# Optimization experiments

Measured on AMD Instinct MI355X. Metric: run time of the kernel, lower is better.

Reference implementation:

```python
import jax, jax.numpy as jnp
import numpy as np

N = 100000   # nodes
E = 1600000  # edges
B = 4096     # graphs
F_IN = 92
H = 51       # hidden_channels
ED = 10      # edge_dim
T = 7        # num_timesteps

def _p(key, shape, scale=0.1):
    return scale * jax.random.normal(key, shape, dtype=jnp.float32)

def setup_inputs():
    key = jax.random.key(0)
    ks = jax.random.split(key, 20)
    return {
        "x": jax.random.normal(ks[0], (N, F_IN), dtype=jnp.float32),
        "edge_index": jax.random.randint(ks[1], (2, E), 0, N),
        "edge_attr": jax.random.normal(ks[2], (E, ED), dtype=jnp.float32),
        "batch": jnp.sort(jax.random.randint(ks[3], (N,), 0, B)),
        "W1": _p(ks[4], (F_IN, H)), "b1": jnp.zeros((H,), jnp.float32),
        "We1": _p(ks[5], (H + ED, H)),
        "att_l": _p(ks[6], (H,)), "att_r": _p(ks[7], (H,)),
        "We2": _p(ks[8], (H, H)), "gate_bias": jnp.zeros((H,), jnp.float32),
        "Wih1": _p(ks[9], (H, 3 * H)), "bih1": jnp.zeros((3 * H,), jnp.float32),
        "Whh1": _p(ks[10], (H, 3 * H)), "bhh1": jnp.zeros((3 * H,), jnp.float32),
        "Wm": _p(ks[11], (H, H)),
        "att_src": _p(ks[12], (H,)), "att_dst": _p(ks[13], (H,)),
        "mol_bias": jnp.zeros((H,), jnp.float32),
        "Wih2": _p(ks[14], (H, 3 * H)), "bih2": jnp.zeros((3 * H,), jnp.float32),
        "Whh2": _p(ks[15], (H, 3 * H)), "bhh2": jnp.zeros((3 * H,), jnp.float32),
        "W2": _p(ks[16], (H, 1)), "b2": jnp.zeros((1,), jnp.float32),
    }

def _lrelu(v):
    return jax.nn.leaky_relu(v, 0.01)

def _seg_softmax(a, idx, num):
    # scatter-softmax over segments (PyG softmax with 1e-16 denom eps)
    m = jax.ops.segment_max(a, idx, num_segments=num)
    e = jnp.exp(a - m[idx])
    s = jax.ops.segment_sum(e, idx, num_segments=num)
    return e / (s[idx] + 1e-16)

def _gru(xin, h, Wih, bih, Whh, bhh):
    # torch.nn.GRUCell, gate order r, z, n
    gi = xin @ Wih + bih
    gh = h @ Whh + bhh
    ir, iz, inn = jnp.split(gi, 3, axis=-1)
    hr, hz, hn = jnp.split(gh, 3, axis=-1)
    r = jax.nn.sigmoid(ir + hr)
    z = jax.nn.sigmoid(iz + hz)
    n = jnp.tanh(inn + r * hn)
    return (1.0 - z) * n + z * h

def reference(x, edge_index, edge_attr, batch, W1, b1, We1, att_l, att_r, We2,
              gate_bias, Wih1, bih1, Whh1, bhh1, Wm, att_src, att_dst, mol_bias,
              Wih2, bih2, Whh2, bhh2, W2, b2):
    src, dst = edge_index[0], edge_index[1]
    # AttentiveFP.lin1 + leaky_relu
    x = _lrelu(x @ W1 + b1)                                        # (N, H)
    # GATEConv: edge-conditioned attention, aggregate to dst
    xe = _lrelu(jnp.concatenate([x[src], edge_attr], axis=-1) @ We1)  # (E, H)
    a = _lrelu(xe @ att_l + x[dst] @ att_r)                        # (E,)
    alpha = _seg_softmax(a, dst, N)
    h = jax.ops.segment_sum((xe @ We2) * alpha[:, None], dst, num_segments=N) + gate_bias
    h = jax.nn.elu(h)                                              # dropout off (eval)
    x = jax.nn.relu(_gru(h, x, Wih1, bih1, Whh1, bhh1))            # (N, H)
    # molecule readout: GATConv over bipartite (nodes -> graphs) edges (arange(N), batch)
    out = jax.nn.relu(jax.ops.segment_sum(x, batch, num_segments=B))  # (B, H)
    xl = x @ Wm                                                    # (N, H), constant over t
    al = xl @ att_src                                              # (N,)
    for _ in range(T):
        ar = (out @ Wm) @ att_dst                                  # (B,)
        a = _lrelu(al + ar[batch])
        alpha = _seg_softmax(a, batch, B)
        hm = jax.ops.segment_sum(xl * alpha[:, None], batch, num_segments=B) + mol_bias
        hm = jax.nn.elu(hm)
        out = jax.nn.relu(_gru(hm, out, Wih2, bih2, Whh2, bhh2))
    return out @ W2 + b2                                           # (B, 1)
```

## Files before the change

kernel.cpp:

```cpp
#include <hip/hip_runtime.h>
#include <stdint.h>

#define NN 100000
#define NE 1600000
#define NB 4096
#define FIN 92
#define H 51
#define H3 153
#define TSTEPS 7
#define SCAN_B 391

__device__ __align__(16) float g_x1[(size_t)NN * 52 + 64];
__device__ __align__(16) float g_p[(size_t)NN * 52 + 64];
__device__ float g_xr[NN];
__device__ float g_agg[(size_t)NN * H + 64];
__device__ float g_x2[(size_t)NN * H + 64];
__device__ float g_xl[(size_t)NN * H + 64];
__device__ float g_al[NN];
__device__ int   g_gs[NB + 2];
__device__ float g_wg1[H * H * 8];
__device__ float g_bg1[64 * 8];
__device__ float g_wg2[H * H * 8];
__device__ float g_bg2[64 * 8];
__device__ float g_wv[64];
__device__ int   g_cnt[NN];
__device__ int   g_rp[NN + 1];
__device__ int   g_cur[NN];
__device__ int   g_src[NE + 4];
__device__ __align__(16) float g_eac[(size_t)NE * 12 + 16];
__device__ int   g_bsum[512];
__device__ int   g_boff[512];

__device__ __forceinline__ float lrelu(float v) { return v > 0.f ? v : 0.01f * v; }
__device__ __forceinline__ float elu1(float v) { return v > 0.f ? v : expm1f(v); }
__device__ __forceinline__ float sigm(float v) { return 1.f / (1.f + __expf(-v)); }

__device__ __forceinline__ float bflo(uint32_t w) { union { uint32_t u; float f; } c; c.u = w << 16; return c.f; }
__device__ __forceinline__ float bfhi(uint32_t w) { union { uint32_t u; float f; } c; c.u = w & 0xffff0000u; return c.f; }
__device__ __forceinline__ uint32_t f2bf(float f) {
    uint32_t u = __float_as_uint(f);
    return (u + 0x7FFFu + ((u >> 16) & 1u)) >> 16;
}

__device__ __forceinline__ float wave_sum(float v) {
    v += __shfl_xor(v, 32, 64);
    v += __shfl_xor(v, 16, 64);
    v += __shfl_xor(v, 8, 64);
    v += __shfl_xor(v, 4, 64);
    v += __shfl_xor(v, 2, 64);
    v += __shfl_xor(v, 1, 64);
    return v;
}
__device__ __forceinline__ void wave_sum4(float& a, float& b, float& c, float& d) {
    a += __shfl_xor(a, 32, 64); b += __shfl_xor(b, 32, 64); c += __shfl_xor(c, 32, 64); d += __shfl_xor(d, 32, 64);
    a += __shfl_xor(a, 16, 64); b += __shfl_xor(b, 16, 64); c += __shfl_xor(c, 16, 64); d += __shfl_xor(d, 16, 64);
    a += __shfl_xor(a, 8, 64);  b += __shfl_xor(b, 8, 64);  c += __shfl_xor(c, 8, 64);  d += __shfl_xor(d, 8, 64);
    a += __shfl_xor(a, 4, 64);  b += __shfl_xor(b, 4, 64);  c += __shfl_xor(c, 4, 64);  d += __shfl_xor(d, 4, 64);
    a += __shfl_xor(a, 2, 64);  b += __shfl_xor(b, 2, 64);  c += __shfl_xor(c, 2, 64);  d += __shfl_xor(d, 2, 64);
    a += __shfl_xor(a, 1, 64);  b += __shfl_xor(b, 1, 64);  c += __shfl_xor(c, 1, 64);  d += __shfl_xor(d, 1, 64);
}

__device__ __forceinline__ float d4(float acc, float4 t, float4 wv) {
    return fmaf(t.x, wv.x, fmaf(t.y, wv.y, fmaf(t.z, wv.z, fmaf(t.w, wv.w, acc))));
}

__global__ __launch_bounds__(256) void k_init(const int* __restrict__ batch) {
    int n = blockIdx.x * 256 + threadIdx.x;
    if (n >= NN) return;
    g_cnt[n] = 0;
    int bn = batch[n];
    int bp = (n == 0) ? -1 : batch[n - 1];
    for (int b = bp + 1; b <= bn; ++b) g_gs[b] = n;
    if (n == NN - 1) for (int b = bn + 1; b <= NB; ++b) g_gs[b] = NN;
}

__global__ void k_prep(const float* __restrict__ Wih1, const float* __restrict__ bih1,
                       const float* __restrict__ Whh1, const float* __restrict__ bhh1,
                       const float* __restrict__ Wih2, const float* __restrict__ bih2,
                       const float* __restrict__ Whh2, const float* __restrict__ bhh2,
                       const float* __restrict__ Wm, const float* __restrict__ ad) {
    int id = blockIdx.x * 256 + threadIdx.x;
    int which = 0;
    const float *Wih, *bih, *Whh, *bhh;
    if (id < H * H) {
        which = 0; Wih = Wih1; bih = bih1; Whh = Whh1; bhh = bhh1;
    } else if (id < 2 * H * H) {
        which = 1; id -= H * H; Wih = Wih2; bih = bih2; Whh = Whh2; bhh = bhh2;
    } else {
        int k = id - 2 * H * H;
        if (k < 64) {
            float a = 0.f;
            if (k < H) for (int j = 0; j < H; ++j) a = fmaf(Wm[k * H + j], ad[j], a);
            g_wv[k] = a;
        }
        return;
    }
    float* Wg = which ? g_wg2 : g_wg1;
    float* bg = which ? g_bg2 : g_bg1;
    int k = id / H, j = id - k * H;
    float* o = Wg + (size_t)id * 8;
    o[0] = Wih[k * H3 + j];
    o[1] = Wih[k * H3 + H + j];
    o[2] = Wih[k * H3 + 2 * H + j];
    o[3] = Whh[k * H3 + j];
    o[4] = Whh[k * H3 + H + j];
    o[5] = Whh[k * H3 + 2 * H + j];
    o[6] = 0.f; o[7] = 0.f;
    if (id < H) {
        float* ob = bg + (size_t)id * 8;
        ob[0] = bih[id]; ob[1] = bih[H + id]; ob[2] = bih[2 * H + id];
        ob[3] = bhh[id]; ob[4] = bhh[H + id]; ob[5] = bhh[2 * H + id];
        ob[6] = 0.f; ob[7] = 0.f;
    }
}

__global__ __launch_bounds__(256) void k_count(const int* __restrict__ ei) {
    int e = blockIdx.x * 256 + threadIdx.x;
    if (e >= NE) return;
    atomicAdd(&g_cnt[ei[NE + e]], 1);
}

__global__ __launch_bounds__(256) void k_scan1() {
    __shared__ int sm[256];
    int tid = threadIdx.x;
    int i = blockIdx.x * 256 + tid;
    sm[tid] = (i < NN) ? g_cnt[i] : 0;
    __syncthreads();
#pragma unroll
    for (int off = 1; off < 256; off <<= 1) {
        int t = (tid >= off) ? sm[tid - off] : 0;
        __syncthreads();
        sm[tid] += t;
        __syncthreads();
    }
    if (i < NN) g_rp[i + 1] = sm[tid];
    if (tid == 255) g_bsum[blockIdx.x] = sm[255];
}

__global__ void k_scan2() {
    __shared__ int sm[512];
    int tid = threadIdx.x;
    sm[tid] = (tid < SCAN_B) ? g_bsum[tid] : 0;
    __syncthreads();
#pragma unroll
    for (int off = 1; off < 512; off <<= 1) {
        int t = (tid >= off) ? sm[tid - off] : 0;
        __syncthreads();
        sm[tid] += t;
        __syncthreads();
    }
    if (tid < SCAN_B) g_boff[tid] = (tid == 0) ? 0 : sm[tid - 1];
}

__global__ __launch_bounds__(256) void k_scan3() {
    int i = blockIdx.x * 256 + threadIdx.x;
    if (i >= NN) return;
    int v = g_rp[i + 1] + g_boff[blockIdx.x];
    g_rp[i + 1] = v;
    if (i == 0) { g_rp[0] = 0; g_cur[0] = 0; }
    if (i + 1 < NN) g_cur[i + 1] = v;
}

__global__ __launch_bounds__(256) void k_fill(const int* __restrict__ ei, const float* __restrict__ ea) {
    int e = blockIdx.x * 256 + threadIdx.x;
    if (e >= NE) return;
    int d = ei[NE + e];
    int pos = atomicAdd(&g_cur[d], 1);
    g_src[pos] = ei[e];
    const float2* s2 = (const float2*)(ea + (size_t)e * 10);
    float2 v0 = s2[0], v1 = s2[1], v2 = s2[2], v3 = s2[3], v4 = s2[4];
    float2* d2 = (float2*)(g_eac + (size_t)pos * 12);
    d2[0] = v0; d2[1] = v1; d2[2] = v2; d2[3] = v3; d2[4] = v4;
    d2[5] = make_float2(0.f, 0.f);
}

__global__ __launch_bounds__(256, 3) void k_lin1(const float* __restrict__ x, const float* __restrict__ W1,
                                                 const float* __restrict__ b1, const float* __restrict__ attr_,
                                                 const float* __restrict__ We1) {
    int n = blockIdx.x * 256 + threadIdx.x;
    if (n >= NN) return;
    const float4* xq4 = (const float4*)(x + (size_t)n * FIN);
    float acc[H];
#pragma unroll
    for (int h = 0; h < H; ++h) acc[h] = 0.f;
#pragma unroll 1
    for (int q = 0; q < FIN / 4; ++q) {
        float4 v = xq4[q];
        const float* wr = W1 + (4 * q) * H;
#pragma unroll
        for (int h = 0; h < H; ++h)
            acc[h] = fmaf(v.x, wr[h], fmaf(v.y, wr[H + h], fmaf(v.z, wr[2 * H + h], fmaf(v.w, wr[3 * H + h], acc[h]))));
    }
    float xrv = 0.f;
    float* xo = g_x1 + (size_t)n * 52;
#pragma unroll
    for (int h = 0; h < H; ++h) {
        float v = lrelu(acc[h] + b1[h]);
        acc[h] = v;
        xo[h] = v;
        xrv = fmaf(v, attr_[h], xrv);
    }
    xo[H] = 0.f;
    g_xr[n] = xrv;
    float* po = g_p + (size_t)n * 52;
#pragma unroll 1
    for (int h = 0; h < H; ++h) {
        float ph = 0.f;
#pragma unroll
        for (int k = 0; k < H; ++k) ph = fmaf(acc[k], We1[k * H + h], ph);
        po[h] = ph;
    }
    po[H] = 0.f;
}

#define MKE(q) make_float4( \
    (4*(q)+0) < 10 ? We1[(51 + 4*(q)+0) * H + lj] : 0.f, \
    (4*(q)+1) < 10 ? We1[(51 + 4*(q)+1) * H + lj] : 0.f, \
    (4*(q)+2) < 10 ? We1[(51 + 4*(q)+2) * H + lj] : 0.f, \
    (4*(q)+3) < 10 ? We1[(51 + 4*(q)+3) * H + lj] : 0.f)

__global__ __launch_bounds__(256, 4) void k_gate(const float* __restrict__ We1, const float* __restrict__ attl) {
    int lane = threadIdx.x & 63;
    int lj = lane < H ? lane : H - 1;
    int n = __builtin_amdgcn_readfirstlane(blockIdx.x * 4 + (threadIdx.x >> 6));
    float4 eq0 = MKE(0), eq1 = MKE(1), eq2 = MKE(2);
    float attlv = attl[lj];
    float xrd = g_xr[n];
    int rs = g_rp[n], re = g_rp[n + 1];
    float accH = 0.f, den = 0.f;
    int nb = (re - rs) >> 2;
    int idx = rs;
    float pv0 = 0.f, pv1 = 0.f, pv2 = 0.f, pv3 = 0.f;
    if (nb > 0) {
        int s0 = __builtin_amdgcn_readfirstlane(g_src[idx]);
        int s1 = __builtin_amdgcn_readfirstlane(g_src[idx + 1]);
        int s2 = __builtin_amdgcn_readfirstlane(g_src[idx + 2]);
        int s3 = __builtin_amdgcn_readfirstlane(g_src[idx + 3]);
        pv0 = g_p[(size_t)s0 * 52 + lane];
        pv1 = g_p[(size_t)s1 * 52 + lane];
        pv2 = g_p[(size_t)s2 * 52 + lane];
        pv3 = g_p[(size_t)s3 * 52 + lane];
    }
#pragma unroll 1
    for (int blk = 0; blk < nb; ++blk) {
        int ci = idx;
        float cp0 = pv0, cp1 = pv1, cp2 = pv2, cp3 = pv3;
        idx += 4;
        if (blk + 1 < nb) {
            int s0 = __builtin_amdgcn_readfirstlane(g_src[idx]);
            int s1 = __builtin_amdgcn_readfirstlane(g_src[idx + 1]);
            int s2 = __builtin_amdgcn_readfirstlane(g_src[idx + 2]);
            int s3 = __builtin_amdgcn_readfirstlane(g_src[idx + 3]);
            pv0 = g_p[(size_t)s0 * 52 + lane];
            pv1 = g_p[(size_t)s1 * 52 + lane];
            pv2 = g_p[(size_t)s2 * 52 + lane];
            pv3 = g_p[(size_t)s3 * 52 + lane];
        }
        const float4* ep0 = (const float4*)(g_eac + (size_t)ci * 12);
        const float4* ep1 = (const float4*)(g_eac + (size_t)(ci + 1) * 12);
        const float4* ep2 = (const float4*)(g_eac + (size_t)(ci + 2) * 12);
        const float4* ep3 = (const float4*)(g_eac + (size_t)(ci + 3) * 12);
        float xe0 = cp0, xe1 = cp1, xe2 = cp2, xe3 = cp3;
        xe0 = d4(xe0, ep0[0], eq0); xe0 = d4(xe0, ep0[1], eq1); xe0 = d4(xe0, ep0[2], eq2);
        xe1 = d4(xe1, ep1[0], eq0); xe1 = d4(xe1, ep1[1], eq1); xe1 = d4(xe1, ep1[2], eq2);
        xe2 = d4(xe2, ep2[0], eq0); xe2 = d4(xe2, ep2[1], eq1); xe2 = d4(xe2, ep2[2], eq2);
        xe3 = d4(xe3, ep3[0], eq0); xe3 = d4(xe3, ep3[1], eq1); xe3 = d4(xe3, ep3[2], eq2);
        float l0 = lrelu(xe0), l1 = lrelu(xe1), l2 = lrelu(xe2), l3 = lrelu(xe3);
        float p0 = (lane < H) ? l0 * attlv : 0.f;
        float p1 = (lane < H) ? l1 * attlv : 0.f;
        float p2 = (lane < H) ? l2 * attlv : 0.f;
        float p3 = (lane < H) ? l3 * attlv : 0.f;
        wave_sum4(p0, p1, p2, p3);
        float e0 = __expf(lrelu(p0 + xrd));
        float e1 = __expf(lrelu(p1 + xrd));
        float e2 = __expf(lrelu(p2 + xrd));
        float e3 = __expf(lrelu(p3 + xrd));
        accH = fmaf(e0, l0, accH); den += e0;
        accH = fmaf(e1, l1, accH); den += e1;
        accH = fmaf(e2, l2, accH); den += e2;
        accH = fmaf(e3, l3, accH); den += e3;
    }
    for (; idx < re; ++idx) {
        int s0 = __builtin_amdgcn_readfirstlane(g_src[idx]);
        float pvs = g_p[(size_t)s0 * 52 + lane];
        const float4* ep0 = (const float4*)(g_eac + (size_t)idx * 12);
        float xe0 = pvs;
        xe0 = d4(xe0, ep0[0], eq0); xe0 = d4(xe0, ep0[1], eq1); xe0 = d4(xe0, ep0[2], eq2);
        float l0 = lrelu(xe0);
        float a0 = wave_sum((lane < H) ? l0 * attlv : 0.f);
        float e0 = __expf(lrelu(a0 + xrd));
        accH = fmaf(e0, l0, accH); den += e0;
    }
    if (lane < H) g_agg[(size_t)n * H + lane] = accH / (den + 1e-16f);
}

__global__ __launch_bounds__(256) void k_gategru(const float* __restrict__ We2, const float* __restrict__ gb,
                                                 const float* __restrict__ Wm, const float* __restrict__ asrc) {
    __shared__ float lbc[4][52][8];
    int w = threadIdx.x >> 6;
    int lane = threadIdx.x & 63;
    int lj = lane < H ? lane : H - 1;
    int base = __builtin_amdgcn_readfirstlane(blockIdx.x * 32 + w * 8);
    float xj[8];
#pragma unroll
    for (int m = 0; m < 8; ++m) xj[m] = g_x1[(size_t)(base + m) * 52 + lane];
    float ac[8];
#pragma unroll
    for (int m = 0; m < 8; ++m) ac[m] = 0.f;
#pragma unroll 2
    for (int k = 0; k < H; ++k) {
        float wv = We2[k * H + lj];
#pragma unroll
        for (int m = 0; m < 8; ++m)
            ac[m] = fmaf(g_agg[(size_t)(base + m) * H + k], wv, ac[m]);
    }
    float gbl = gb[lj];
    float hb[8];
#pragma unroll
    for (int m = 0; m < 8; ++m) hb[m] = elu1(ac[m] + gbl);
    if (lane < H) {
#pragma unroll
        for (int m = 0; m < 8; ++m) lbc[w][lane][m] = hb[m];
    }
    float gir[8], giz[8], gin[8], ghr[8], ghz[8], ghn[8];
#pragma unroll
    for (int m = 0; m < 8; ++m) { gir[m] = 0; giz[m] = 0; gin[m] = 0; ghr[m] = 0; ghz[m] = 0; ghn[m] = 0; }
#pragma unroll 2
    for (int k = 0; k < H; ++k) {
        const float4* wp = (const float4*)(g_wg1 + ((size_t)(k * H + lj)) * 8);
        float4 w0 = wp[0];
        float4 w1 = wp[1];
        float4 h0 = *(const float4*)&lbc[w][k][0];
        float4 h1 = *(const float4*)&lbc[w][k][4];
        float hk[8] = { h0.x, h0.y, h0.z, h0.w, h1.x, h1.y, h1.z, h1.w };
#pragma unroll
        for (int m = 0; m < 8; ++m) {
            float xk = g_x1[(size_t)(base + m) * 52 + k];
            gir[m] = fmaf(hk[m], w0.x, gir[m]); giz[m] = fmaf(hk[m], w0.y, giz[m]); gin[m] = fmaf(hk[m], w0.z, gin[m]);
            ghr[m] = fmaf(xk, w0.w, ghr[m]);    ghz[m] = fmaf(xk, w1.x, ghz[m]);    ghn[m] = fmaf(xk, w1.y, ghn[m]);
        }
    }
    const float4* bp = (const float4*)(g_bg1 + lane * 8);
    float4 b0 = bp[0];
    float4 b1v = bp[1];
    float o2[8];
#pragma unroll
    for (int m = 0; m < 8; ++m) {
        float r = sigm(gir[m] + b0.x + ghr[m] + b0.w);
        float z = sigm(giz[m] + b0.y + ghz[m] + b1v.x);
        float nn2 = tanhf(gin[m] + b0.z + r * (ghn[m] + b1v.y));
        o2[m] = fmaxf((1.f - z) * nn2 + z * xj[m], 0.f);
        if (lane < H) g_x2[(size_t)(base + m) * H + lane] = o2[m];
    }
    if (lane < H) {
#pragma unroll
        for (int m = 0; m < 8; ++m) lbc[w][lane][m] = o2[m];
    }
    float xl[8];
#pragma unroll
    for (int m = 0; m < 8; ++m) xl[m] = 0.f;
#pragma unroll 2
    for (int k = 0; k < H; ++k) {
        float wv = Wm[k * H + lj];
        float4 o0 = *(const float4*)&lbc[w][k][0];
        float4 o1 = *(const float4*)&lbc[w][k][4];
        xl[0] = fmaf(o0.x, wv, xl[0]); xl[1] = fmaf(o0.y, wv, xl[1]);
        xl[2] = fmaf(o0.z, wv, xl[2]); xl[3] = fmaf(o0.w, wv, xl[3]);
        xl[4] = fmaf(o1.x, wv, xl[4]); xl[5] = fmaf(o1.y, wv, xl[5]);
        xl[6] = fmaf(o1.z, wv, xl[6]); xl[7] = fmaf(o1.w, wv, xl[7]);
    }
    float asl = asrc[lj];
    float v0, v1, v2, v3, v4, v5, v6, v7;
    v0 = (lane < H) ? xl[0] * asl : 0.f;
    v1 = (lane < H) ? xl[1] * asl : 0.f;
    v2 = (lane < H) ? xl[2] * asl : 0.f;
    v3 = (lane < H) ? xl[3] * asl : 0.f;
    v4 = (lane < H) ? xl[4] * asl : 0.f;
    v5 = (lane < H) ? xl[5] * asl : 0.f;
    v6 = (lane < H) ? xl[6] * asl : 0.f;
    v7 = (lane < H) ? xl[7] * asl : 0.f;
    wave_sum4(v0, v1, v2, v3);
    wave_sum4(v4, v5, v6, v7);
#pragma unroll
    for (int m = 0; m < 8; ++m)
        if (lane < H) g_xl[(size_t)(base + m) * H + lane] = xl[m];
    if (lane == 0) {
        g_al[base + 0] = v0; g_al[base + 1] = v1; g_al[base + 2] = v2; g_al[base + 3] = v3;
        g_al[base + 4] = v4; g_al[base + 5] = v5; g_al[base + 6] = v6; g_al[base + 7] = v7;
    }
}

__global__ __launch_bounds__(256) void k_mol_all(const float* __restrict__ mb, const float* __restrict__ W2,
                                                 const float* __restrict__ b2, float* __restrict__ dout) {
    __shared__ uint32_t ldsWa[H * H];
    __shared__ uint32_t ldsWb[H * H];
    __shared__ uint32_t ldsWc[H * H];
    __shared__ float lbc[4][52][2];
    int tid = threadIdx.x;
    for (int i = tid; i < H * H; i += 256) {
        const float* s = g_wg2 + (size_t)i * 8;
        ldsWa[i] = f2bf(s[0]) | (f2bf(s[1]) << 16);
        ldsWb[i] = f2bf(s[2]) | (f2bf(s[3]) << 16);
        ldsWc[i] = f2bf(s[4]) | (f2bf(s[5]) << 16);
    }
    __syncthreads();
    int w = tid >> 6;
    int lane = tid & 63;
    int lj = lane < H ? lane : H - 1;
    int b = __builtin_amdgcn_readfirstlane(blockIdx.x * 4 + w);
    int gs = g_gs[b], ge = g_gs[b + 1];
    float oa = 0.f, ob = 0.f;
    int i = gs;
    for (; i + 2 <= ge; i += 2) {
        oa += g_x2[(size_t)i * H + lane];
        ob += g_x2[(size_t)(i + 1) * H + lane];
    }
    if (i < ge) oa += g_x2[(size_t)i * H + lane];
    float oj = fmaxf(oa + ob, 0.f);
    float wvl = g_wv[lane];
    float mbl = mb[lj];
    const float4* bp = (const float4*)(g_bg2 + lane * 8);
    float4 b0 = bp[0];
    float4 b1v = bp[1];
#pragma unroll 1
    for (int t = 0; t < TSTEPS; ++t) {
        float arb = wave_sum((lane < H) ? oj * wvl : 0.f);
        float sa = 0.f, sb = 0.f, aa = 0.f, ab = 0.f;
        i = gs;
        for (; i + 2 <= ge; i += 2) {
            float ev0 = __expf(lrelu(g_al[i] + arb));
            float ev1 = __expf(lrelu(g_al[i + 1] + arb));
            sa += ev0; sb += ev1;
            aa = fmaf(ev0, g_xl[(size_t)i * H + lane], aa);
            ab = fmaf(ev1, g_xl[(size_t)(i + 1) * H + lane], ab);
        }
        if (i < ge) {
            float ev0 = __expf(lrelu(g_al[i] + arb));
            sa += ev0;
            aa = fmaf(ev0, g_xl[(size_t)i * H + lane], aa);
        }
        float inv = 1.f / (sa + sb + 1e-16f);
        float hm = elu1((aa + ab) * inv + mbl);
        if (lane < H) { lbc[w][lane][0] = hm; lbc[w][lane][1] = oj; }
        float gir = 0, giz = 0, gin = 0, ghr = 0, ghz = 0, ghn = 0;
#pragma unroll 2
        for (int k = 0; k < H; ++k) {
            uint32_t wa = ldsWa[k * H + lj];
            uint32_t wb = ldsWb[k * H + lj];
            uint32_t wc = ldsWc[k * H + lj];
            float2 ho = *(const float2*)&lbc[w][k][0];
            float hmk = ho.x, ok = ho.y;
            gir = fmaf(hmk, bflo(wa), gir); giz = fmaf(hmk, bfhi(wa), giz); gin = fmaf(hmk, bflo(wb), gin);
            ghr = fmaf(ok, bfhi(wb), ghr);  ghz = fmaf(ok, bflo(wc), ghz);  ghn = fmaf(ok, bfhi(wc), ghn);
        }
        float r = sigm(gir + b0.x + ghr + b0.w);
        float z = sigm(giz + b0.y + ghz + b1v.x);
        float nn2 = tanhf(gin + b0.z + r * (ghn + b1v.y));
        oj = fmaxf((1.f - z) * nn2 + z * oj, 0.f);
    }
    float fv = wave_sum((lane < H) ? oj * W2[lj] : 0.f);
    if (lane == 0) dout[b] = fv + b2[0];
}

extern "C" void kernel_launch(void* const* d_in, const int* in_sizes, int n_in,
                              void* d_out, int out_size, void* d_ws, size_t ws_size,
                              hipStream_t stream) {
    const float* x     = (const float*)d_in[0];
    const int*   ei    = (const int*)d_in[1];
    const float* ea    = (const float*)d_in[2];
    const int*   batch = (const int*)d_in[3];
    const float* W1    = (const float*)d_in[4];
    const float* b1    = (const float*)d_in[5];
    const float* We1   = (const float*)d_in[6];
    const float* attl  = (const float*)d_in[7];
    const float* attr_ = (const float*)d_in[8];
    const float* We2   = (const float*)d_in[9];
    const float* gb    = (const float*)d_in[10];
    const float* Wm    = (const float*)d_in[15];
    const float* asrc  = (const float*)d_in[16];
    const float* adst  = (const float*)d_in[17];
    const float* mb    = (const float*)d_in[18];
    const float* W2    = (const float*)d_in[23];
    const float* b2    = (const float*)d_in[24];
    float* dout = (float*)d_out;

    k_init<<<SCAN_B, 256, 0, stream>>>(batch);
    k_count<<<NE / 256, 256, 0, stream>>>(ei);
    k_scan1<<<SCAN_B, 256, 0, stream>>>();
    k_scan2<<<1, 512, 0, stream>>>();
    k_scan3<<<SCAN_B, 256, 0, stream>>>();
    k_fill<<<NE / 256, 256, 0, stream>>>(ei, ea);

    k_prep<<<(2 * H * H + 64 + 255) / 256, 256, 0, stream>>>(
        (const float*)d_in[11], (const float*)d_in[12], (const float*)d_in[13], (const float*)d_in[14],
        (const float*)d_in[19], (const float*)d_in[20], (const float*)d_in[21], (const float*)d_in[22],
        Wm, adst);

    k_lin1<<<(NN + 255) / 256, 256, 0, stream>>>(x, W1, b1, attr_, We1);
    k_gate<<<NN / 4, 256, 0, stream>>>(We1, attl);
    k_gategru<<<NN / 32, 256, 0, stream>>>(We2, gb, Wm, asrc);
    k_mol_all<<<NB / 4, 256, 0, stream>>>(mb, W2, b2, dout);
}
```

Baseline: 657.2 us.

## Stage GRU weights as bf16 in LDS and make gate-GRU kernel persistent

The gate+GRU node kernel now runs as a persistent grid of 1024 blocks that loop over 32-node chunks. Each block first packs the six GRU weight columns into bf16 pairs in shared memory, which replaces the per-iteration global float4 weight loads. It also sets the inner loops to unroll 1. The bf16 weights lower the precision of the GRU1 matmul and add conversion ALU work, and the large LDS footprint may cut occupancy.

```diff
diff --git a/kernel.cpp b/kernel.cpp
--- a/kernel.cpp
+++ b/kernel.cpp
@@ -9,6 +9,8 @@
 #define H3 153
 #define TSTEPS 7
 #define SCAN_B 391
+#define GG_BLOCKS 1024
+#define GG_CHUNKS (NN / 32)
 
 __device__ __align__(16) float g_x1[(size_t)NN * 52 + 64];
 __device__ __align__(16) float g_p[(size_t)NN * 52 + 64];
@@ -296,97 +298,113 @@
 
 __global__ __launch_bounds__(256) void k_gategru(const float* __restrict__ We2, const float* __restrict__ gb,
                                                  const float* __restrict__ Wm, const float* __restrict__ asrc) {
+    __shared__ uint32_t wA[H * H];
+    __shared__ uint32_t wB[H * H];
+    __shared__ uint32_t wC[H * H];
     __shared__ float lbc[4][52][8];
-    int w = threadIdx.x >> 6;
-    int lane = threadIdx.x & 63;
+    int tid = threadIdx.x;
+    for (int i = tid; i < H * H; i += 256) {
+        const float* s = g_wg1 + (size_t)i * 8;
+        wA[i] = f2bf(s[0]) | (f2bf(s[1]) << 16);
+        wB[i] = f2bf(s[2]) | (f2bf(s[3]) << 16);
+        wC[i] = f2bf(s[4]) | (f2bf(s[5]) << 16);
+    }
+    __syncthreads();
+    int w = tid >> 6;
+    int lane = tid & 63;
     int lj = lane < H ? lane : H - 1;
-    int base = __builtin_amdgcn_readfirstlane(blockIdx.x * 32 + w * 8);
-    float xj[8];
-#pragma unroll
-    for (int m = 0; m < 8; ++m) xj[m] = g_x1[(size_t)(base + m) * 52 + lane];
-    float ac[8];
-#pragma unroll
-    for (int m = 0; m < 8; ++m) ac[m] = 0.f;
-#pragma unroll 2
-    for (int k = 0; k < H; ++k) {
-        float wv = We2[k * H + lj];
-#pragma unroll
-        for (int m = 0; m < 8; ++m)
-            ac[m] = fmaf(g_agg[(size_t)(base + m) * H + k], wv, ac[m]);
-    }
-    float gbl = gb[lj];
-    float hb[8];
-#pragma unroll
-    for (int m = 0; m < 8; ++m) hb[m] = elu1(ac[m] + gbl);
-    if (lane < H) {
-#pragma unroll
-        for (int m = 0; m < 8; ++m) lbc[w][lane][m] = hb[m];
-    }
-    float gir[8], giz[8], gin[8], ghr[8], ghz[8], ghn[8];
-#pragma unroll
-    for (int m = 0; m < 8; ++m) { gir[m] = 0; giz[m] = 0; gin[m] = 0; ghr[m] = 0; ghz[m] = 0; ghn[m] = 0; }
-#pragma unroll 2
-    for (int k = 0; k < H; ++k) {
-        const float4* wp = (const float4*)(g_wg1 + ((size_t)(k * H + lj)) * 8);
-        float4 w0 = wp[0];
-        float4 w1 = wp[1];
-        float4 h0 = *(const float4*)&lbc[w][k][0];
-        float4 h1 = *(const float4*)&lbc[w][k][4];
-        float hk[8] = { h0.x, h0.y, h0.z, h0.w, h1.x, h1.y, h1.z, h1.w };
-#pragma unroll
-        for (int m = 0; m < 8; ++m) {
-            float xk = g_x1[(size_t)(base + m) * 52 + k];
-            gir[m] = fmaf(hk[m], w0.x, gir[m]); giz[m] = fmaf(hk[m], w0.y, giz[m]); gin[m] = fmaf(hk[m], w0.z, gin[m]);
-            ghr[m] = fmaf(xk, w0.w, ghr[m]);    ghz[m] = fmaf(xk, w1.x, ghz[m]);    ghn[m] = fmaf(xk, w1.y, ghn[m]);
-        }
-    }
     const float4* bp = (const float4*)(g_bg1 + lane * 8);
     float4 b0 = bp[0];
     float4 b1v = bp[1];
-    float o2[8];
-#pragma unroll
-    for (int m = 0; m < 8; ++m) {
-        float r = sigm(gir[m] + b0.x + ghr[m] + b0.w);
-        float z = sigm(giz[m] + b0.y + ghz[m] + b1v.x);
-        float nn2 = tanhf(gin[m] + b0.z + r * (ghn[m] + b1v.y));
-        o2[m] = fmaxf((1.f - z) * nn2 + z * xj[m], 0.f);
-        if (lane < H) g_x2[(size_t)(base + m) * H + lane] = o2[m];
-    }
-    if (lane < H) {
-#pragma unroll
-        for (int m = 0; m < 8; ++m) lbc[w][lane][m] = o2[m];
-    }
-    float xl[8];
-#pragma unroll
-    for (int m = 0; m < 8; ++m) xl[m] = 0.f;
-#pragma unroll 2
-    for (int k = 0; k < H; ++k) {
-        float wv = Wm[k * H + lj];
-        float4 o0 = *(const float4*)&lbc[w][k][0];
-        float4 o1 = *(const float4*)&lbc[w][k][4];
-        xl[0] = fmaf(o0.x, wv, xl[0]); xl[1] = fmaf(o0.y, wv, xl[1]);
-        xl[2] = fmaf(o0.z, wv, xl[2]); xl[3] = fmaf(o0.w, wv, xl[3]);
-        xl[4] = fmaf(o1.x, wv, xl[4]); xl[5] = fmaf(o1.y, wv, xl[5]);
-        xl[6] = fmaf(o1.z, wv, xl[6]); xl[7] = fmaf(o1.w, wv, xl[7]);
-    }
+    float gbl = gb[lj];
     float asl = asrc[lj];
-    float v0, v1, v2, v3, v4, v5, v6, v7;
-    v0 = (lane < H) ? xl[0] * asl : 0.f;
-    v1 = (lane < H) ? xl[1] * asl : 0.f;
-    v2 = (lane < H) ? xl[2] * asl : 0.f;
-    v3 = (lane < H) ? xl[3] * asl : 0.f;
-    v4 = (lane < H) ? xl[4] * asl : 0.f;
-    v5 = (lane < H) ? xl[5] * asl : 0.f;
-    v6 = (lane < H) ? xl[6] * asl : 0.f;
-    v7 = (lane < H) ? xl[7] * asl : 0.f;
-    wave_sum4(v0, v1, v2, v3);
-    wave_sum4(v4, v5, v6, v7);
-#pragma unroll
-    for (int m = 0; m < 8; ++m)
-        if (lane < H) g_xl[(size_t)(base + m) * H + lane] = xl[m];
-    if (lane == 0) {
-        g_al[base + 0] = v0; g_al[base + 1] = v1; g_al[base + 2] = v2; g_al[base + 3] = v3;
-        g_al[base + 4] = v4; g_al[base + 5] = v5; g_al[base + 6] = v6; g_al[base + 7] = v7;
+#pragma unroll 1
+    for (int chunk = blockIdx.x; chunk < GG_CHUNKS; chunk += GG_BLOCKS) {
+        int base = __builtin_amdgcn_readfirstlane(chunk * 32 + w * 8);
+        float xj[8];
+#pragma unroll
+        for (int m = 0; m < 8; ++m) xj[m] = g_x1[(size_t)(base + m) * 52 + lane];
+        float ac[8];
+#pragma unroll
+        for (int m = 0; m < 8; ++m) ac[m] = 0.f;
+#pragma unroll 1
+        for (int k = 0; k < H; ++k) {
+            float wv = We2[k * H + lj];
+#pragma unroll
+            for (int m = 0; m < 8; ++m)
+                ac[m] = fmaf(g_agg[(size_t)(base + m) * H + k], wv, ac[m]);
+        }
+        float hb[8];
+#pragma unroll
+        for (int m = 0; m < 8; ++m) hb[m] = elu1(ac[m] + gbl);
+        if (lane < H) {
+#pragma unroll
+            for (int m = 0; m < 8; ++m) lbc[w][lane][m] = hb[m];
+        }
+        float gir[8], giz[8], gin[8], ghr[8], ghz[8], ghn[8];
+#pragma unroll
+        for (int m = 0; m < 8; ++m) { gir[m] = 0; giz[m] = 0; gin[m] = 0; ghr[m] = 0; ghz[m] = 0; ghn[m] = 0; }
+#pragma unroll 1
+        for (int k = 0; k < H; ++k) {
+            uint32_t wa = wA[k * H + lj];
+            uint32_t wb = wB[k * H + lj];
+            uint32_t wc = wC[k * H + lj];
+            float w0x = bflo(wa), w0y = bfhi(wa), w0z = bflo(wb);
+            float w0w = bfhi(wb), w1x = bflo(wc), w1y = bfhi(wc);
+            float4 h0 = *(const float4*)&lbc[w][k][0];
+            float4 h1 = *(const float4*)&lbc[w][k][4];
+            float hk[8] = { h0.x, h0.y, h0.z, h0.w, h1.x, h1.y, h1.z, h1.w };
+#pragma unroll
+            for (int m = 0; m < 8; ++m) {
+                float xk = g_x1[(size_t)(base + m) * 52 + k];
+                gir[m] = fmaf(hk[m], w0x, gir[m]); giz[m] = fmaf(hk[m], w0y, giz[m]); gin[m] = fmaf(hk[m], w0z, gin[m]);
+                ghr[m] = fmaf(xk, w0w, ghr[m]);    ghz[m] = fmaf(xk, w1x, ghz[m]);    ghn[m] = fmaf(xk, w1y, ghn[m]);
+            }
+        }
+        float o2[8];
+#pragma unroll
+        for (int m = 0; m < 8; ++m) {
+            float r = sigm(gir[m] + b0.x + ghr[m] + b0.w);
+            float z = sigm(giz[m] + b0.y + ghz[m] + b1v.x);
+            float nn2 = tanhf(gin[m] + b0.z + r * (ghn[m] + b1v.y));
+            o2[m] = fmaxf((1.f - z) * nn2 + z * xj[m], 0.f);
+            if (lane < H) g_x2[(size_t)(base + m) * H + lane] = o2[m];
+        }
+        if (lane < H) {
+#pragma unroll
+            for (int m = 0; m < 8; ++m) lbc[w][lane][m] = o2[m];
+        }
+        float xl[8];
+#pragma unroll
+        for (int m = 0; m < 8; ++m) xl[m] = 0.f;
+#pragma unroll 1
+        for (int k = 0; k < H; ++k) {
+            float wv = Wm[k * H + lj];
+            float4 o0 = *(const float4*)&lbc[w][k][0];
+            float4 o1 = *(const float4*)&lbc[w][k][4];
+            xl[0] = fmaf(o0.x, wv, xl[0]); xl[1] = fmaf(o0.y, wv, xl[1]);
+            xl[2] = fmaf(o0.z, wv, xl[2]); xl[3] = fmaf(o0.w, wv, xl[3]);
+            xl[4] = fmaf(o1.x, wv, xl[4]); xl[5] = fmaf(o1.y, wv, xl[5]);
+            xl[6] = fmaf(o1.z, wv, xl[6]); xl[7] = fmaf(o1.w, wv, xl[7]);
+        }
+        float v0, v1, v2, v3, v4, v5, v6, v7;
+        v0 = (lane < H) ? xl[0] * asl : 0.f;
+        v1 = (lane < H) ? xl[1] * asl : 0.f;
+        v2 = (lane < H) ? xl[2] * asl : 0.f;
+        v3 = (lane < H) ? xl[3] * asl : 0.f;
+        v4 = (lane < H) ? xl[4] * asl : 0.f;
+        v5 = (lane < H) ? xl[5] * asl : 0.f;
+        v6 = (lane < H) ? xl[6] * asl : 0.f;
+        v7 = (lane < H) ? xl[7] * asl : 0.f;
+        wave_sum4(v0, v1, v2, v3);
+        wave_sum4(v4, v5, v6, v7);
+#pragma unroll
+        for (int m = 0; m < 8; ++m)
+            if (lane < H) g_xl[(size_t)(base + m) * H + lane] = xl[m];
+        if (lane == 0) {
+            g_al[base + 0] = v0; g_al[base + 1] = v1; g_al[base + 2] = v2; g_al[base + 3] = v3;
+            g_al[base + 4] = v4; g_al[base + 5] = v5; g_al[base + 6] = v6; g_al[base + 7] = v7;
+        }
     }
 }
 
@@ -498,6 +516,6 @@
 
     k_lin1<<<(NN + 255) / 256, 256, 0, stream>>>(x, W1, b1, attr_, We1);
     k_gate<<<NN / 4, 256, 0, stream>>>(We1, attl);
-    k_gategru<<<NN / 32, 256, 0, stream>>>(We2, gb, Wm, asrc);
+    k_gategru<<<GG_BLOCKS, 256, 0, stream>>>(We2, gb, Wm, asrc);
     k_mol_all<<<NB / 4, 256, 0, stream>>>(mb, W2, b2, dout);
 }
```

Measured after the change: 659.4 us. About the same (+0.3%).
